# Kernel tuning notes

Hardware: AMD Instinct MI355X
Metric: run time of the kernel (lower is better)

Reference implementation:

```python
import jax, jax.numpy as jnp
import numpy as np

B, LT, LS, D, H, F = 4, 1024, 1024, 1024, 16, 4096
HD = D // H
EPS = 1e-6


def rms_norm(x, g):
    return x / jnp.sqrt(jnp.mean(x * x, axis=-1, keepdims=True) + EPS) * g


def mha(q_in, kv_in, wq, wk, wv, wo, bias):
    # q_in: [B,Lq,D], kv_in: [B,Lk,D], bias broadcastable to [B,H,Lq,Lk]
    b, lq, _ = q_in.shape
    lk = kv_in.shape[1]
    q = (q_in @ wq).reshape(b, lq, H, HD).transpose(0, 2, 1, 3)
    k = (kv_in @ wk).reshape(b, lk, H, HD).transpose(0, 2, 1, 3)
    v = (kv_in @ wv).reshape(b, lk, H, HD).transpose(0, 2, 1, 3)
    s = jnp.einsum('bhqd,bhkd->bhqk', q, k) / np.sqrt(HD).astype(np.float32) + bias
    o = jnp.einsum('bhqk,bhkd->bhqd', jax.nn.softmax(s, axis=-1), v)
    o = o.transpose(0, 2, 1, 3).reshape(b, lq, D) @ wo
    return o, k, v


def setup_inputs() -> dict:
    key = jax.random.key(0)
    ks = jax.random.split(key, 16)
    f = lambda k, sh, s: jax.random.normal(k, sh, jnp.float32) * s
    wscale = 1.0 / float(np.sqrt(D))
    causal = jnp.where(jnp.triu(jnp.ones((LT, LT), bool), 1), jnp.float32(-1e9), jnp.float32(0.0))
    return {
        'x': f(ks[0], (B, LT, D), 1.0),
        'memory': f(ks[1], (B, LS, D), 1.0),
        'position_embedding': f(ks[2], (1, H, LT, LS), 0.02),
        'causal_mask': causal,
        'gamma_sa': jnp.ones((D,), jnp.float32),
        'wq_s': f(ks[3], (D, D), wscale), 'wk_s': f(ks[4], (D, D), wscale),
        'wv_s': f(ks[5], (D, D), wscale), 'wo_s': f(ks[6], (D, D), wscale),
        'gamma_ca': jnp.ones((D,), jnp.float32),
        'wq_c': f(ks[7], (D, D), wscale), 'wk_c': f(ks[8], (D, D), wscale),
        'wv_c': f(ks[9], (D, D), wscale), 'wo_c': f(ks[10], (D, D), wscale),
        'gamma_m': jnp.ones((D,), jnp.float32),
        'w1': f(ks[11], (D, F), wscale), 'w2': f(ks[12], (F, D), 1.0 / float(np.sqrt(F))),
    }


def reference(x, memory, position_embedding, causal_mask,
              gamma_sa, wq_s, wk_s, wv_s, wo_s,
              gamma_ca, wq_c, wk_c, wv_c, wo_c,
              gamma_m, w1, w2):
    # self-attention block (pre-RMSNorm, causal mask, residual)
    h = rms_norm(x, gamma_sa)
    a, k_s, v_s = mha(h, h, wq_s, wk_s, wv_s, wo_s, causal_mask[None, None, :, :])
    attn_x = a + x
    # cross-attention block (position-embedding bias on scores, residual)
    h2 = rms_norm(attn_x, gamma_ca)
    c, k_c, v_c = mha(h2, memory, wq_c, wk_c, wv_c, wo_c, position_embedding)
    cross_x = c + attn_x
    # FFN block
    h3 = rms_norm(cross_x, gamma_m)
    mlp_x = jax.nn.relu(h3 @ w1) @ w2 + cross_x
    return mlp_x, (k_s, v_s), (k_c, v_c)
```

## Files before the change

### kernel.cpp

```cpp
#include <hip/hip_runtime.h>
#include <stdint.h>
#include <stddef.h>

typedef __bf16 bf16_t;
typedef __attribute__((ext_vector_type(8))) __bf16 bf16x8;
typedef __attribute__((ext_vector_type(4))) __bf16 bf16x4;
typedef __attribute__((ext_vector_type(4))) float f32x4;

#define LT 1024
#define LS 1024
#define DM 1024
#define NH 16
#define HD 64
#define FF 4096
#define BB 4

__device__ __forceinline__ void gld_lds16(const bf16_t* g, bf16_t* l) {
    __builtin_amdgcn_global_load_lds(
        (const __attribute__((address_space(1))) void*)g,
        (__attribute__((address_space(3))) void*)l, 16, 0, 0);
}

__global__ __launch_bounds__(256) void transpose_f2bf(
    const float* __restrict__ in, bf16_t* __restrict__ out, int R, int C)
{
    __shared__ float tile[32][33];
    int bx = blockIdx.x * 32;
    int by = blockIdx.y * 32;
    int tx = threadIdx.x, ty = threadIdx.y;
#pragma unroll
    for (int j = 0; j < 4; j++)
        tile[ty + j * 8][tx] = in[(size_t)(by + ty + j * 8) * C + bx + tx];
    __syncthreads();
#pragma unroll
    for (int j = 0; j < 4; j++)
        out[(size_t)(bx + ty + j * 8) * R + by + tx] = (bf16_t)tile[tx][ty + j * 8];
}

struct TPtrs { const float* in[8]; bf16_t* out[8]; };
__global__ __launch_bounds__(256) void transpose8_f2bf(TPtrs p)
{
    __shared__ float tile[32][33];
    const float* in = p.in[blockIdx.z];
    bf16_t* out = p.out[blockIdx.z];
    int bx = blockIdx.x * 32;
    int by = blockIdx.y * 32;
    int tx = threadIdx.x, ty = threadIdx.y;
#pragma unroll
    for (int j = 0; j < 4; j++)
        tile[ty + j * 8][tx] = in[(size_t)(by + ty + j * 8) * 1024 + bx + tx];
    __syncthreads();
#pragma unroll
    for (int j = 0; j < 4; j++)
        out[(size_t)(bx + ty + j * 8) * 1024 + by + tx] = (bf16_t)tile[tx][ty + j * 8];
}

__global__ __launch_bounds__(256) void transpose_bf(
    const bf16_t* __restrict__ in, bf16_t* __restrict__ out)
{
    __shared__ bf16_t tile[32][33];
    int bh = blockIdx.z;
    int r0 = blockIdx.x * 32;
    int c0 = blockIdx.y * 32;
    const bf16_t* ib = in + (size_t)bh * LT * HD;
    bf16_t* ob = out + (size_t)bh * HD * LT;
    int tx = threadIdx.x, ty = threadIdx.y;
#pragma unroll
    for (int j = 0; j < 4; j++)
        tile[ty + j * 8][tx] = ib[(size_t)(r0 + ty + j * 8) * HD + c0 + tx];
    __syncthreads();
#pragma unroll
    for (int j = 0; j < 4; j++)
        ob[(size_t)(c0 + ty + j * 8) * LT + r0 + tx] = tile[tx][ty + j * 8];
}

__global__ __launch_bounds__(256) void f2bf_kernel(
    const float* __restrict__ in, bf16_t* __restrict__ out, size_t n)
{
    size_t i = ((size_t)blockIdx.x * 256 + threadIdx.x) * 4;
    if (i + 3 < n) {
        float4 v = *(const float4*)&in[i];
        out[i + 0] = (bf16_t)v.x;
        out[i + 1] = (bf16_t)v.y;
        out[i + 2] = (bf16_t)v.z;
        out[i + 3] = (bf16_t)v.w;
    }
}

__global__ __launch_bounds__(256) void reduce2_res(
    const float* __restrict__ p, const float* __restrict__ res,
    float* __restrict__ out)
{
    const size_t MN = (size_t)BB * LT * DM;
    size_t i = ((size_t)blockIdx.x * 256 + threadIdx.x) * 4;
    float4 a = *(const float4*)&p[i];
    float4 b = *(const float4*)&p[i + MN];
    float4 r = *(const float4*)&res[i];
    float4 o;
    o.x = a.x + b.x + r.x; o.y = a.y + b.y + r.y;
    o.z = a.z + b.z + r.z; o.w = a.w + b.w + r.w;
    *(float4*)&out[i] = o;
}

__global__ __launch_bounds__(256) void rmsnorm_kernel(
    const float* __restrict__ x, const float* __restrict__ g,
    bf16_t* __restrict__ out)
{
    __shared__ float red[4];
    int row = blockIdx.x;
    int t = threadIdx.x;
    int lane = t & 63, w = t >> 6;
    const float* xr = x + (size_t)row * DM;
    float4 v = *(const float4*)&xr[t * 4];
    float ss = v.x * v.x + v.y * v.y + v.z * v.z + v.w * v.w;
#pragma unroll
    for (int off = 32; off > 0; off >>= 1) ss += __shfl_down(ss, off, 64);
    if (lane == 0) red[w] = ss;
    __syncthreads();
    float tot = red[0] + red[1] + red[2] + red[3];
    float inv = rsqrtf(tot * (1.0f / DM) + 1e-6f);
    float4 gv = *(const float4*)&g[t * 4];
    bf16_t* o = out + (size_t)row * DM + t * 4;
    o[0] = (bf16_t)(v.x * inv * gv.x);
    o[1] = (bf16_t)(v.y * inv * gv.y);
    o[2] = (bf16_t)(v.z * inv * gv.z);
    o[3] = (bf16_t)(v.w * inv * gv.w);
}

#define GEMM_BODY(Aptr, Btptr, Kstride, kBeg, kEnd)                              \
    for (int k0 = (kBeg); k0 < (kEnd); k0 += 64) {                               \
        __syncthreads();                                                         \
        _Pragma("unroll")                                                        \
        for (int i = 0; i < 4; i++) {                                            \
            int p = i * 256 + t;                                                 \
            int row = p >> 3;                                                    \
            int g = (p & 7) ^ (row & 7);                                         \
            gld_lds16(&(Aptr)[(size_t)(m0 + row) * (Kstride) + k0 + g * 8],      \
                      &lA[p * 8]);                                               \
            gld_lds16(&(Btptr)[(size_t)(n0 + row) * (Kstride) + k0 + g * 8],     \
                      &lB[p * 8]);                                               \
        }                                                                        \
        __syncthreads();                                                         \
        _Pragma("unroll")                                                        \
        for (int s = 0; s < 2; s++) {                                            \
            bf16x8 af[4], bfr[4];                                                \
            _Pragma("unroll")                                                    \
            for (int mt = 0; mt < 4; mt++) {                                     \
                int r = wr * 64 + mt * 16 + l15;                                 \
                af[mt] = *(const bf16x8*)&lA[((r << 3) + ((s * 4 + quad) ^ (r & 7))) << 3]; \
            }                                                                    \
            _Pragma("unroll")                                                    \
            for (int nt = 0; nt < 4; nt++) {                                     \
                int r = wc * 64 + nt * 16 + l15;                                 \
                bfr[nt] = *(const bf16x8*)&lB[((r << 3) + ((s * 4 + quad) ^ (r & 7))) << 3]; \
            }                                                                    \
            _Pragma("unroll")                                                    \
            for (int mt = 0; mt < 4; mt++)                                       \
                _Pragma("unroll")                                                \
                for (int nt = 0; nt < 4; nt++)                                   \
                    acc[mt][nt] = __builtin_amdgcn_mfma_f32_16x16x32_bf16(       \
                        af[mt], bfr[nt], acc[mt][nt], 0, 0, 0);                  \
        }                                                                        \
    }

__global__ __launch_bounds__(256) void gemm_qkv(
    const bf16_t* __restrict__ A1, const bf16_t* __restrict__ B1, int nb1,
    const bf16_t* __restrict__ A2, const bf16_t* __restrict__ B2, int secbase2,
    bf16_t* __restrict__ qb,
    float* __restrict__ kF, bf16_t* __restrict__ kB,
    float* __restrict__ vF, bf16_t* __restrict__ vB)
{
    __shared__ bf16_t lA[128 * 64];
    __shared__ bf16_t lB[128 * 64];
    const int t = threadIdx.x;
    const int lane = t & 63, w = t >> 6;
    const int quad = lane >> 4, l15 = lane & 15;
    const int m0 = blockIdx.x * 128;
    const int wr = w >> 1, wc = w & 1;

    const bf16_t* A; const bf16_t* Bt; int n0, sec0;
    if ((int)blockIdx.y < nb1) { A = A1; Bt = B1; n0 = blockIdx.y * 128; sec0 = 0; }
    else { A = A2; Bt = B2; n0 = (blockIdx.y - nb1) * 128; sec0 = secbase2; }

    f32x4 acc[4][4] = {};
    GEMM_BODY(A, Bt, 1024, 0, 1024)

#pragma unroll
    for (int mt = 0; mt < 4; mt++) {
#pragma unroll
        for (int nt = 0; nt < 4; nt++) {
#pragma unroll
            for (int r = 0; r < 4; r++) {
                int row = m0 + wr * 64 + mt * 16 + quad * 4 + r;
                int col = n0 + wc * 64 + nt * 16 + l15;
                float v = acc[mt][nt][r];
                int b = row >> 10, tp = row & 1023;
                int sec = sec0 + (col >> 10);
                int c10 = col & 1023;
                int h = c10 >> 6, d = c10 & 63;
                size_t idx = (((size_t)(b * NH + h)) << 16) + (size_t)tp * HD + d;
                if (sec == 0) {
                    qb[idx] = (bf16_t)v;
                } else if (sec == 1) {
                    kF[idx] = v;
                    kB[idx] = (bf16_t)v;
                } else {
                    vF[idx] = v;
                    vB[idx] = (bf16_t)v;
                }
            }
        }
    }
}

#define EP_RES 0
#define EP_RELU 1
#define EP_PART 2

template <int EP, int KSPLIT>
__global__ __launch_bounds__(256) void gemm_bt(
    const bf16_t* __restrict__ A, const bf16_t* __restrict__ Bt,
    int N, int K,
    float* __restrict__ outF, const float* __restrict__ res,
    bf16_t* __restrict__ outB)
{
    __shared__ bf16_t lA[128 * 64];
    __shared__ bf16_t lB[128 * 64];
    const int t = threadIdx.x;
    const int lane = t & 63, w = t >> 6;
    const int quad = lane >> 4, l15 = lane & 15;
    const int m0 = blockIdx.x * 128, n0 = blockIdx.y * 128;
    const int wr = w >> 1, wc = w & 1;
    const int Kc = K / KSPLIT;
    const int kBeg = blockIdx.z * Kc;

    f32x4 acc[4][4] = {};
    GEMM_BODY(A, Bt, K, kBeg, kBeg + Kc)

    float* dst = outF;
    if constexpr (EP == EP_PART)
        dst = outF + (size_t)blockIdx.z * (size_t)gridDim.x * 128 * N;

#pragma unroll
    for (int mt = 0; mt < 4; mt++) {
#pragma unroll
        for (int nt = 0; nt < 4; nt++) {
#pragma unroll
            for (int r = 0; r < 4; r++) {
                int row = m0 + wr * 64 + mt * 16 + quad * 4 + r;
                int col = n0 + wc * 64 + nt * 16 + l15;
                float v = acc[mt][nt][r];
                if constexpr (EP == EP_RES) {
                    dst[(size_t)row * N + col] = v + res[(size_t)row * N + col];
                } else if constexpr (EP == EP_RELU) {
                    outB[(size_t)row * N + col] = (bf16_t)fmaxf(v, 0.0f);
                } else {
                    dst[(size_t)row * N + col] = v;
                }
            }
        }
    }
}

template <bool CAUSAL>
__global__ __launch_bounds__(256, 4) void flash_attn(
    const bf16_t* __restrict__ Q, const bf16_t* __restrict__ Kb,
    const bf16_t* __restrict__ Vt, const float* __restrict__ bias,
    bf16_t* __restrict__ O)
{
    __shared__ bf16_t lK[2][64 * 64];
    __shared__ bf16_t lV[2][64 * 64];
    __shared__ bf16_t lP[4][16 * 64];
    const int t = threadIdx.x;
    const int lane = t & 63, w = t >> 6;
    const int quad = lane >> 4, l15 = lane & 15;
    const int qt = blockIdx.x;
    const int yy = blockIdx.y;
    const int h = yy >> 2, b = yy & 3;
    const int bhd = b * NH + h;
    const int q0 = qt * 64;

    const bf16_t* qbase = Q + (size_t)bhd * LT * HD;
    const bf16_t* kbase = Kb + (size_t)bhd * LS * HD;
    const bf16_t* vbase = Vt + (size_t)bhd * HD * LS;
    const float* bbase = bias + (size_t)h * LT * LS;

    bf16x8 qf[2];
    const int qrow = q0 + w * 16 + l15;
#pragma unroll
    for (int s = 0; s < 2; s++)
        qf[s] = *(const bf16x8*)&qbase[(size_t)qrow * HD + s * 32 + quad * 8];

    f32x4 acc_o[4] = {};
    float m_i = -3.0e38f, l_i = 0.0f;

    const int nkt = CAUSAL ? (qt + 1) : (LS / 64);

    float bnxt[16], bcur[16];
    if constexpr (!CAUSAL) {
#pragma unroll
        for (int nt = 0; nt < 4; nt++)
#pragma unroll
            for (int r = 0; r < 4; r++)
                bnxt[nt * 4 + r] =
                    bbase[(size_t)qrow * LS + nt * 16 + quad * 4 + r];
    }
#pragma unroll
    for (int i = 0; i < 2; i++) {
        int p = i * 256 + t;
        int row = p >> 3;
        int g = (p & 7) ^ (row & 7);
        gld_lds16(&kbase[(size_t)row * HD + g * 8], &lK[0][p * 8]);
        gld_lds16(&vbase[(size_t)row * LS + g * 8], &lV[0][p * 8]);
    }

    for (int kt = 0; kt < nkt; kt++) {
        const int d = kt & 1;
        const int nxt = kt + 1;
        if constexpr (!CAUSAL) {
#pragma unroll
            for (int i = 0; i < 16; i++) bcur[i] = bnxt[i];
        }
        if (nxt < nkt) {
            const int nb = nxt * 64;
            const int nd = nxt & 1;
            if constexpr (!CAUSAL) {
#pragma unroll
                for (int nt = 0; nt < 4; nt++)
#pragma unroll
                    for (int r = 0; r < 4; r++)
                        bnxt[nt * 4 + r] =
                            bbase[(size_t)qrow * LS + nb + nt * 16 + quad * 4 + r];
            }
#pragma unroll
            for (int i = 0; i < 2; i++) {
                int p = i * 256 + t;
                int row = p >> 3;
                int g = (p & 7) ^ (row & 7);
                gld_lds16(&kbase[(size_t)(nb + row) * HD + g * 8], &lK[nd][p * 8]);
                gld_lds16(&vbase[(size_t)row * LS + nb + g * 8], &lV[nd][p * 8]);
            }
            if constexpr (!CAUSAL) {
                asm volatile("s_waitcnt vmcnt(20)" ::: "memory");
            } else {
                asm volatile("s_waitcnt vmcnt(4)" ::: "memory");
            }
        } else {
            asm volatile("s_waitcnt vmcnt(0)" ::: "memory");
        }
        __builtin_amdgcn_s_barrier();
        __builtin_amdgcn_sched_barrier(0);

        const int kb = kt * 64;

        f32x4 sacc[4];
        __builtin_amdgcn_s_setprio(1);
#pragma unroll
        for (int nt = 0; nt < 4; nt++) {
            f32x4 sa = {};
#pragma unroll
            for (int s = 0; s < 2; s++) {
                int r = nt * 16 + l15;
                bf16x8 kf = *(const bf16x8*)&lK[d][((r << 3) + ((s * 4 + quad) ^ (r & 7))) << 3];
                sa = __builtin_amdgcn_mfma_f32_16x16x32_bf16(kf, qf[s], sa, 0, 0, 0);
            }
            sacc[nt] = sa;
        }
        __builtin_amdgcn_s_setprio(0);

        float sval[4][4];
        float tmn[4];
#pragma unroll
        for (int nt = 0; nt < 4; nt++) {
#pragma unroll
            for (int r = 0; r < 4; r++) {
                float v = sacc[nt][r] * 0.125f;
                if constexpr (CAUSAL) {
                    int col = kb + nt * 16 + quad * 4 + r;
                    if (col > qrow) v = -1e9f;
                } else {
                    v += bcur[nt * 4 + r];
                }
                sval[nt][r] = v;
            }
            tmn[nt] = fmaxf(fmaxf(sval[nt][0], sval[nt][1]),
                            fmaxf(sval[nt][2], sval[nt][3]));
        }
        float tm = fmaxf(fmaxf(tmn[0], tmn[1]), fmaxf(tmn[2], tmn[3]));
        tm = fmaxf(tm, __shfl_xor(tm, 16, 64));
        tm = fmaxf(tm, __shfl_xor(tm, 32, 64));

        if (!__all(tm <= m_i + 8.0f)) {
            float mn = fmaxf(m_i, tm);
            float alpha = __expf(m_i - mn);
            m_i = mn;
            l_i *= alpha;
            float ar[4];
#pragma unroll
            for (int r = 0; r < 4; r++) ar[r] = __shfl(alpha, quad * 4 + r, 64);
#pragma unroll
            for (int dt = 0; dt < 4; dt++)
#pragma unroll
                for (int r = 0; r < 4; r++) acc_o[dt][r] *= ar[r];
        }

        float rs[4];
#pragma unroll
        for (int nt = 0; nt < 4; nt++) {
            float p0 = __expf(sval[nt][0] - m_i);
            float p1 = __expf(sval[nt][1] - m_i);
            float p2 = __expf(sval[nt][2] - m_i);
            float p3 = __expf(sval[nt][3] - m_i);
            rs[nt] = (p0 + p1) + (p2 + p3);
            bf16x4 pk;
            pk[0] = (bf16_t)p0; pk[1] = (bf16_t)p1;
            pk[2] = (bf16_t)p2; pk[3] = (bf16_t)p3;
            int gc = nt * 2 + (quad >> 1);
            int eoff = ((l15 << 3) + (gc ^ (l15 & 7))) * 8 + (quad & 1) * 4;
            *(bf16x4*)&lP[w][eoff] = pk;
        }
        float rsum = (rs[0] + rs[1]) + (rs[2] + rs[3]);
        rsum += __shfl_xor(rsum, 16, 64);
        rsum += __shfl_xor(rsum, 32, 64);
        l_i += rsum;

#pragma unroll
        for (int s = 0; s < 2; s++) {
            bf16x8 pf = *(const bf16x8*)&lP[w][((l15 << 3) + ((s * 4 + quad) ^ (l15 & 7))) << 3];
            __builtin_amdgcn_s_setprio(1);
#pragma unroll
            for (int dt = 0; dt < 4; dt++) {
                int r = dt * 16 + l15;
                bf16x8 vf = *(const bf16x8*)&lV[d][((r << 3) + ((s * 4 + quad) ^ (r & 7))) << 3];
                acc_o[dt] = __builtin_amdgcn_mfma_f32_16x16x32_bf16(pf, vf, acc_o[dt], 0, 0, 0);
            }
            __builtin_amdgcn_s_setprio(0);
        }
        __builtin_amdgcn_s_barrier();
    }

    float lr[4];
#pragma unroll
    for (int r = 0; r < 4; r++) lr[r] = __shfl(l_i, quad * 4 + r, 64);
#pragma unroll
    for (int dt = 0; dt < 4; dt++) {
#pragma unroll
        for (int r = 0; r < 4; r++) {
            int row = q0 + w * 16 + quad * 4 + r;
            int col = h * HD + dt * 16 + l15;
            float v = acc_o[dt][r] / lr[r];
            O[((size_t)(b * LT + row)) * DM + col] = (bf16_t)v;
        }
    }
}

extern "C" void kernel_launch(void* const* d_in, const int* in_sizes, int n_in,
                              void* d_out, int out_size, void* d_ws, size_t ws_size,
                              hipStream_t stream)
{
    (void)in_sizes; (void)n_in; (void)out_size; (void)ws_size;
    const float* x    = (const float*)d_in[0];
    const float* mem  = (const float*)d_in[1];
    const float* pemb = (const float*)d_in[2];
    const float* g_sa = (const float*)d_in[4];
    const float* wq_s = (const float*)d_in[5];
    const float* wk_s = (const float*)d_in[6];
    const float* wv_s = (const float*)d_in[7];
    const float* wo_s = (const float*)d_in[8];
    const float* g_ca = (const float*)d_in[9];
    const float* wq_c = (const float*)d_in[10];
    const float* wk_c = (const float*)d_in[11];
    const float* wv_c = (const float*)d_in[12];
    const float* wo_c = (const float*)d_in[13];
    const float* g_m  = (const float*)d_in[14];
    const float* w1   = (const float*)d_in[15];
    const float* w2   = (const float*)d_in[16];
    float* out = (float*)d_out;

    const size_t OFF_KS = 4u * 1024 * 1024;
    const size_t OFF_VS = 8u * 1024 * 1024;
    const size_t OFF_KC = 12u * 1024 * 1024;
    const size_t OFF_VC = 16u * 1024 * 1024;

    char* ws = (char*)d_ws;
    const size_t MB = 1024 * 1024;
    bf16_t* wqkvTs = (bf16_t*)(ws + 0 * MB);
    bf16_t* woTs   = (bf16_t*)(ws + 6 * MB);
    bf16_t* wqTc   = (bf16_t*)(ws + 8 * MB);
    bf16_t* wkvTc  = (bf16_t*)(ws + 10 * MB);
    bf16_t* woTc   = (bf16_t*)(ws + 14 * MB);
    bf16_t* w1T    = (bf16_t*)(ws + 16 * MB);
    bf16_t* w2T    = (bf16_t*)(ws + 24 * MB);
    bf16_t* membf  = (bf16_t*)(ws + 32 * MB);
    bf16_t* hbuf   = (bf16_t*)(ws + 40 * MB);
    bf16_t* qbuf   = (bf16_t*)(ws + 48 * MB);
    bf16_t* kbuf   = (bf16_t*)(ws + 56 * MB);
    bf16_t* vbuf   = (bf16_t*)(ws + 64 * MB);
    bf16_t* vTbuf  = (bf16_t*)(ws + 72 * MB);
    bf16_t* Obuf   = (bf16_t*)(ws + 80 * MB);
    float*  attn_x  = (float*)(ws + 88 * MB);
    float*  cross_x = (float*)(ws + 112 * MB);
    bf16_t* ffnmid  = (bf16_t*)(ws + 48 * MB);
    float*  part    = (float*)(ws + 80 * MB);

    dim3 tb(32, 8);
    TPtrs tp;
    tp.in[0] = wq_s; tp.out[0] = wqkvTs;
    tp.in[1] = wk_s; tp.out[1] = wqkvTs + 1024 * 1024;
    tp.in[2] = wv_s; tp.out[2] = wqkvTs + 2 * 1024 * 1024;
    tp.in[3] = wo_s; tp.out[3] = woTs;
    tp.in[4] = wq_c; tp.out[4] = wqTc;
    tp.in[5] = wk_c; tp.out[5] = wkvTc;
    tp.in[6] = wv_c; tp.out[6] = wkvTc + 1024 * 1024;
    tp.in[7] = wo_c; tp.out[7] = woTc;
    transpose8_f2bf<<<dim3(32, 32, 8), tb, 0, stream>>>(tp);
    transpose_f2bf<<<dim3(128, 32), tb, 0, stream>>>(w1, w1T, DM, FF);
    transpose_f2bf<<<dim3(32, 128), tb, 0, stream>>>(w2, w2T, FF, DM);

    f2bf_kernel<<<4096, 256, 0, stream>>>(mem, membf, (size_t)BB * LS * DM);

    rmsnorm_kernel<<<BB * LT, 256, 0, stream>>>(x, g_sa, hbuf);
    gemm_qkv<<<dim3(32, 24), 256, 0, stream>>>(
        hbuf, wqkvTs, 24, hbuf, wqkvTs, 0,
        qbuf, out + OFF_KS, kbuf, out + OFF_VS, vbuf);
    transpose_bf<<<dim3(32, 2, 64), tb, 0, stream>>>(vbuf, vTbuf);
    flash_attn<true><<<dim3(16, 64), 256, 0, stream>>>(qbuf, kbuf, vTbuf, nullptr, Obuf);
    gemm_bt<EP_RES, 1><<<dim3(32, 8), 256, 0, stream>>>(
        Obuf, woTs, 1024, 1024, attn_x, x, nullptr);

    rmsnorm_kernel<<<BB * LT, 256, 0, stream>>>(attn_x, g_ca, hbuf);
    gemm_qkv<<<dim3(32, 24), 256, 0, stream>>>(
        hbuf, wqTc, 8, membf, wkvTc, 1,
        qbuf, out + OFF_KC, kbuf, out + OFF_VC, vbuf);
    transpose_bf<<<dim3(32, 2, 64), tb, 0, stream>>>(vbuf, vTbuf);
    flash_attn<false><<<dim3(16, 64), 256, 0, stream>>>(qbuf, kbuf, vTbuf, pemb, Obuf);
    gemm_bt<EP_RES, 1><<<dim3(32, 8), 256, 0, stream>>>(
        Obuf, woTc, 1024, 1024, cross_x, attn_x, nullptr);

    rmsnorm_kernel<<<BB * LT, 256, 0, stream>>>(cross_x, g_m, hbuf);
    gemm_bt<EP_RELU, 1><<<dim3(32, 32), 256, 0, stream>>>(
        hbuf, w1T, 4096, 1024, nullptr, nullptr, ffnmid);
    gemm_bt<EP_PART, 2><<<dim3(32, 8, 2), 256, 0, stream>>>(
        ffnmid, w2T, 1024, 4096, part, nullptr, nullptr);
    reduce2_res<<<4096, 256, 0, stream>>>(part, cross_x, out);
}
```

Before: 600.3 us.

## Fold softmax scale and log2e into Q, use exp2 and defer row-sum reduction

Folds the 1/sqrt(HD) scale and log2(e) into the Q projection epilogue so the attention inner loop can use exp2 directly, with the bias fused via one fma. The causal mask check runs only on the diagonal tile, and the running-max shuffle reduction happens only when the lazy-rescale threshold is exceeded. Row sums stay per lane and are reduced once at the end, with a reciprocal multiply instead of a divide. The P tile in LDS gets a different swizzle, now read as two 4-wide loads. Together these cut VALU and shuffle work per tile. Rounding Q to bf16 after the scale is applied slightly changes numerics.

After: 591.2 us. About the same (-1.5%).

```diff
diff --git a/kernel.cpp b/kernel.cpp
--- a/kernel.cpp
+++ b/kernel.cpp
@@ -14,6 +14,19 @@
 #define HD 64
 #define FF 4096
 #define BB 4
+
+#define LOG2E 1.4426950408889634f
+
+#if __has_builtin(__builtin_amdgcn_exp2f)
+#define EXP2F(x) __builtin_amdgcn_exp2f(x)
+#else
+#define EXP2F(x) exp2f(x)
+#endif
+#if __has_builtin(__builtin_amdgcn_rcpf)
+#define RCPF(x) __builtin_amdgcn_rcpf(x)
+#else
+#define RCPF(x) (1.0f / (x))
+#endif
 
 __device__ __forceinline__ void gld_lds16(const bf16_t* g, bf16_t* l) {
     __builtin_amdgcn_global_load_lds(
@@ -200,7 +213,7 @@
                 int h = c10 >> 6, d = c10 & 63;
                 size_t idx = (((size_t)(b * NH + h)) << 16) + (size_t)tp * HD + d;
                 if (sec == 0) {
-                    qb[idx] = (bf16_t)v;
+                    qb[idx] = (bf16_t)(v * (0.125f * LOG2E));
                 } else if (sec == 1) {
                     kF[idx] = v;
                     kB[idx] = (bf16_t)v;
@@ -274,6 +287,7 @@
     const int t = threadIdx.x;
     const int lane = t & 63, w = t >> 6;
     const int quad = lane >> 4, l15 = lane & 15;
+    const int xr8 = l15 & 7, xb = l15 >> 3;
     const int qt = blockIdx.x;
     const int yy = blockIdx.y;
     const int h = yy >> 2, b = yy & 3;
@@ -292,7 +306,8 @@
         qf[s] = *(const bf16x8*)&qbase[(size_t)qrow * HD + s * 32 + quad * 8];
 
     f32x4 acc_o[4] = {};
-    float m_i = -3.0e38f, l_i = 0.0f;
+    float m2 = -3.0e38f;
+    float lp = 0.0f;
 
     const int nkt = CAUSAL ? (qt + 1) : (LS / 64);
 
@@ -351,8 +366,6 @@
         __builtin_amdgcn_s_barrier();
         __builtin_amdgcn_sched_barrier(0);
 
-        const int kb = kt * 64;
-
         f32x4 sacc[4];
         __builtin_amdgcn_s_setprio(1);
 #pragma unroll
@@ -374,27 +387,30 @@
         for (int nt = 0; nt < 4; nt++) {
 #pragma unroll
             for (int r = 0; r < 4; r++) {
-                float v = sacc[nt][r] * 0.125f;
+                float v = sacc[nt][r];
                 if constexpr (CAUSAL) {
-                    int col = kb + nt * 16 + quad * 4 + r;
-                    if (col > qrow) v = -1e9f;
+                    if (kt == nkt - 1) {
+                        int col = kt * 64 + nt * 16 + quad * 4 + r;
+                        if (col > qrow) v = -1e9f;
+                    }
                 } else {
-                    v += bcur[nt * 4 + r];
+                    v = fmaf(bcur[nt * 4 + r], LOG2E, v);
                 }
                 sval[nt][r] = v;
             }
             tmn[nt] = fmaxf(fmaxf(sval[nt][0], sval[nt][1]),
                             fmaxf(sval[nt][2], sval[nt][3]));
         }
-        float tm = fmaxf(fmaxf(tmn[0], tmn[1]), fmaxf(tmn[2], tmn[3]));
-        tm = fmaxf(tm, __shfl_xor(tm, 16, 64));
-        tm = fmaxf(tm, __shfl_xor(tm, 32, 64));
-
-        if (!__all(tm <= m_i + 8.0f)) {
-            float mn = fmaxf(m_i, tm);
-            float alpha = __expf(m_i - mn);
-            m_i = mn;
-            l_i *= alpha;
+        float pm = fmaxf(fmaxf(tmn[0], tmn[1]), fmaxf(tmn[2], tmn[3]));
+
+        if (!__all(pm <= m2 + 11.5f)) {
+            float tm = pm;
+            tm = fmaxf(tm, __shfl_xor(tm, 16, 64));
+            tm = fmaxf(tm, __shfl_xor(tm, 32, 64));
+            float mn = fmaxf(m2, tm);
+            float alpha = EXP2F(m2 - mn);
+            m2 = mn;
+            lp *= alpha;
             float ar[4];
 #pragma unroll
             for (int r = 0; r < 4; r++) ar[r] = __shfl(alpha, quad * 4 + r, 64);
@@ -404,29 +420,27 @@
                 for (int r = 0; r < 4; r++) acc_o[dt][r] *= ar[r];
         }
 
-        float rs[4];
 #pragma unroll
         for (int nt = 0; nt < 4; nt++) {
-            float p0 = __expf(sval[nt][0] - m_i);
-            float p1 = __expf(sval[nt][1] - m_i);
-            float p2 = __expf(sval[nt][2] - m_i);
-            float p3 = __expf(sval[nt][3] - m_i);
-            rs[nt] = (p0 + p1) + (p2 + p3);
+            float p0 = EXP2F(sval[nt][0] - m2);
+            float p1 = EXP2F(sval[nt][1] - m2);
+            float p2 = EXP2F(sval[nt][2] - m2);
+            float p3 = EXP2F(sval[nt][3] - m2);
+            lp += (p0 + p1) + (p2 + p3);
             bf16x4 pk;
             pk[0] = (bf16_t)p0; pk[1] = (bf16_t)p1;
             pk[2] = (bf16_t)p2; pk[3] = (bf16_t)p3;
             int gc = nt * 2 + (quad >> 1);
-            int eoff = ((l15 << 3) + (gc ^ (l15 & 7))) * 8 + (quad & 1) * 4;
-            *(bf16x4*)&lP[w][eoff] = pk;
-        }
-        float rsum = (rs[0] + rs[1]) + (rs[2] + rs[3]);
-        rsum += __shfl_xor(rsum, 16, 64);
-        rsum += __shfl_xor(rsum, 32, 64);
-        l_i += rsum;
+            int pos = ((gc ^ xr8) << 3) + (((quad & 1) ^ xb) << 2);
+            *(bf16x4*)&lP[w][(l15 << 6) + pos] = pk;
+        }
 
 #pragma unroll
         for (int s = 0; s < 2; s++) {
-            bf16x8 pf = *(const bf16x8*)&lP[w][((l15 << 3) + ((s * 4 + quad) ^ (l15 & 7))) << 3];
+            int gbase = (l15 << 6) + (((s * 4 + quad) ^ xr8) << 3);
+            bf16x4 plo = *(const bf16x4*)&lP[w][gbase + ((0 ^ xb) << 2)];
+            bf16x4 phi = *(const bf16x4*)&lP[w][gbase + ((1 ^ xb) << 2)];
+            bf16x8 pf = __builtin_shufflevector(plo, phi, 0, 1, 2, 3, 4, 5, 6, 7);
             __builtin_amdgcn_s_setprio(1);
 #pragma unroll
             for (int dt = 0; dt < 4; dt++) {
@@ -439,16 +453,19 @@
         __builtin_amdgcn_s_barrier();
     }
 
+    float lf = lp;
+    lf += __shfl_xor(lf, 16, 64);
+    lf += __shfl_xor(lf, 32, 64);
     float lr[4];
 #pragma unroll
-    for (int r = 0; r < 4; r++) lr[r] = __shfl(l_i, quad * 4 + r, 64);
+    for (int r = 0; r < 4; r++) lr[r] = RCPF(__shfl(lf, quad * 4 + r, 64));
 #pragma unroll
     for (int dt = 0; dt < 4; dt++) {
 #pragma unroll
         for (int r = 0; r < 4; r++) {
             int row = q0 + w * 16 + quad * 4 + r;
             int col = h * HD + dt * 16 + l15;
-            float v = acc_o[dt][r] / lr[r];
+            float v = acc_o[dt][r] * lr[r];
             O[((size_t)(b * LT + row)) * DM + col] = (bf16_t)v;
         }
     }
```
